# Kernel optimization log

Hardware: AMD Instinct MI355X
Metric: run time of the kernel (lower is better)

Reference implementation:

```python
import jax, jax.numpy as jnp
import numpy as np

DIM = 128
HEADS = 4
CH = DIM // HEADS  # out_channels per head = 32
EDGE_DIM = 1
N_NODES = 50000
N_EDGES = 800000
NEG_SLOPE = 0.2
LN_EPS = 1e-5
SM_EPS = 1e-16  # PyG softmax denom eps


def setup_inputs() -> dict:
    key = jax.random.key(0)
    ks = jax.random.split(key, 10)
    x = jax.random.normal(ks[0], (N_NODES, DIM), dtype=jnp.float32)
    edge_index = jax.random.randint(ks[1], (2, N_EDGES), 0, N_NODES, dtype=jnp.int64)
    edge_attr = jax.random.normal(ks[2], (N_EDGES, EDGE_DIM), dtype=jnp.float32)
    s = 0.05
    W_l = jax.random.normal(ks[3], (DIM, HEADS * CH), dtype=jnp.float32) * s   # shared lin_l/lin_r (share_weights=True)
    b_l = jax.random.normal(ks[4], (HEADS * CH,), dtype=jnp.float32) * s
    W_e = jax.random.normal(ks[5], (EDGE_DIM, HEADS * CH), dtype=jnp.float32) * s  # lin_edge (no bias)
    att = jax.random.normal(ks[6], (HEADS, CH), dtype=jnp.float32) * s
    bias = jax.random.normal(ks[7], (HEADS * CH,), dtype=jnp.float32) * s      # conv output bias
    ln_gamma = jnp.ones((DIM,), dtype=jnp.float32)
    ln_beta = jnp.zeros((DIM,), dtype=jnp.float32)
    return {"x": x, "edge_index": edge_index, "edge_attr": edge_attr,
            "W_l": W_l, "b_l": b_l, "W_e": W_e, "att": att, "bias": bias,
            "ln_gamma": ln_gamma, "ln_beta": ln_beta}


def reference(x, edge_index, edge_attr, W_l, b_l, W_e, att, bias, ln_gamma, ln_beta):
    N = x.shape[0]
    src, dst = edge_index[0], edge_index[1]

    # --- GATv2Conv (share_weights=True, add_self_loops=False, edge_dim injection) ---
    xl = (x @ W_l + b_l).reshape(N, HEADS, CH)            # [N,H,C] (x_l == x_r)
    e = (edge_attr @ W_e).reshape(-1, HEADS, CH)          # [E,H,C]
    m = jax.nn.leaky_relu(xl[src] + xl[dst] + e, NEG_SLOPE)  # [E,H,C]
    alpha = jnp.einsum('ehc,hc->eh', m, att)              # [E,H]

    # segment softmax over destination node neighborhoods
    amax = jax.ops.segment_max(alpha, dst, num_segments=N)   # [N,H]
    ea = jnp.exp(alpha - amax[dst])                           # [E,H]
    denom = jax.ops.segment_sum(ea, dst, num_segments=N)      # [N,H]
    alpha = ea / (denom[dst] + SM_EPS)

    # scatter-aggregate: sum alpha * x_j (projected source feats)
    out = jax.ops.segment_sum(alpha[:, :, None] * xl[src], dst, num_segments=N)  # [N,H,C]
    h = out.reshape(N, HEADS * CH) + bias                  # concat heads + bias -> [N,dim]

    # --- LayerNorm -> GELU (exact, torch default) -> Dropout(eval=identity) -> residual ---
    mu = h.mean(axis=-1, keepdims=True)
    var = ((h - mu) ** 2).mean(axis=-1, keepdims=True)
    hn = (h - mu) * jax.lax.rsqrt(var + LN_EPS) * ln_gamma + ln_beta
    h = jax.nn.gelu(hn, approximate=False)
    return x + h
```

## Files before the change

kernel.cpp:

```cpp
#include <hip/hip_runtime.h>
#include <hip/hip_bf16.h>
#include <stdint.h>


typedef short bf16x8 __attribute__((ext_vector_type(8)));
typedef float f32x4  __attribute__((ext_vector_type(4)));

__device__ __forceinline__ unsigned int f2bf(float f)
{
    __hip_bfloat16 h = __float2bfloat16(f);
    unsigned short u;
    __builtin_memcpy(&u, &h, 2);
    return (unsigned int)u;
}

__global__ void fill_kernel(float* out, int n, float v)
{
    int i = blockIdx.x * 256 + threadIdx.x;
    if (i < n) out[i] = v;
}

__global__ __launch_bounds__(256) void gemm_xl_kernel(
    const float* __restrict__ x, const float* __restrict__ W,
    const float* __restrict__ b, unsigned int* __restrict__ xl, int N)
{
    __shared__ __align__(16) unsigned short sWt[128 * 136];
    __shared__ __align__(16) unsigned short sOut[4 * 16 * 136];
    int tid = threadIdx.x;

    {
        int c  = tid & 127;
        int kh = tid >> 7;
        const float* Wc = W + (size_t)kh * 64 * 128 + c;
        unsigned short* dst = sWt + c * 136 + kh * 64;
#pragma unroll 4
        for (int kk = 0; kk < 16; ++kk) {
            float w0 = Wc[(kk * 4 + 0) * 128];
            float w1 = Wc[(kk * 4 + 1) * 128];
            float w2 = Wc[(kk * 4 + 2) * 128];
            float w3 = Wc[(kk * 4 + 3) * 128];
            uint2 p;
            p.x = f2bf(w0) | (f2bf(w1) << 16);
            p.y = f2bf(w2) | (f2bf(w3) << 16);
            *(uint2*)(dst + kk * 4) = p;
        }
    }
    __syncthreads();

    int w = tid >> 6, lane = tid & 63;
    int li = lane & 15, g = lane >> 4;
    int n0 = blockIdx.x * 128 + w * 32;

    f32x4 acc[2][8];
#pragma unroll
    for (int nt = 0; nt < 8; ++nt) {
        float bb = b[nt * 16 + li];
#pragma unroll
        for (int mt = 0; mt < 2; ++mt) {
            acc[mt][nt][0] = bb; acc[mt][nt][1] = bb;
            acc[mt][nt][2] = bb; acc[mt][nt][3] = bb;
        }
    }

    int row0 = n0 + li;        if (row0 >= N) row0 = N - 1;
    int row1 = n0 + 16 + li;   if (row1 >= N) row1 = N - 1;
    const float* xr0 = x + (size_t)row0 * 128 + g * 8;
    const float* xr1 = x + (size_t)row1 * 128 + g * 8;

#pragma unroll
    for (int kb = 0; kb < 4; ++kb) {
        union { uint32_t u[4]; bf16x8 v; } A0, A1;
        {
            float4 a  = *(const float4*)(xr0 + kb * 32);
            float4 bq = *(const float4*)(xr0 + kb * 32 + 4);
            A0.u[0] = f2bf(a.x)  | (f2bf(a.y)  << 16);
            A0.u[1] = f2bf(a.z)  | (f2bf(a.w)  << 16);
            A0.u[2] = f2bf(bq.x) | (f2bf(bq.y) << 16);
            A0.u[3] = f2bf(bq.z) | (f2bf(bq.w) << 16);
        }
        {
            float4 a  = *(const float4*)(xr1 + kb * 32);
            float4 bq = *(const float4*)(xr1 + kb * 32 + 4);
            A1.u[0] = f2bf(a.x)  | (f2bf(a.y)  << 16);
            A1.u[1] = f2bf(a.z)  | (f2bf(a.w)  << 16);
            A1.u[2] = f2bf(bq.x) | (f2bf(bq.y) << 16);
            A1.u[3] = f2bf(bq.z) | (f2bf(bq.w) << 16);
        }
        const unsigned short* wb = sWt + kb * 32 + g * 8;
#pragma unroll
        for (int nt = 0; nt < 8; ++nt) {
            bf16x8 Bf = *(const bf16x8*)(wb + (nt * 16 + li) * 136);
            acc[0][nt] = __builtin_amdgcn_mfma_f32_16x16x32_bf16(A0.v, Bf, acc[0][nt], 0, 0, 0);
            acc[1][nt] = __builtin_amdgcn_mfma_f32_16x16x32_bf16(A1.v, Bf, acc[1][nt], 0, 0, 0);
        }
    }

    unsigned short* so = sOut + w * 16 * 136;
#pragma unroll
    for (int mt = 0; mt < 2; ++mt) {
#pragma unroll
        for (int nt = 0; nt < 8; ++nt)
#pragma unroll
            for (int r = 0; r < 4; ++r)
                so[(g * 4 + r) * 136 + nt * 16 + li] =
                    (unsigned short)f2bf(acc[mt][nt][r]);
        int rb = n0 + mt * 16;
        for (int it = 0; it < 16; ++it) {
            int n = rb + it;
            if (n < N)
                xl[(size_t)n * 64 + lane] = *(const uint32_t*)(so + it * 136 + lane * 2);
        }
    }
}

__global__ void rank_kernel(const int* __restrict__ ei, int* __restrict__ deg,
                            int* __restrict__ rank, int E, int N)
{
    int e = blockIdx.x * 256 + threadIdx.x;
    if (e < E) {
        int d = ei[(size_t)E + e];
        if ((unsigned)d >= (unsigned)N) d = 0;
        rank[e] = atomicAdd(&deg[d], 1);
    }
}

__global__ void scan_reduce_kernel(const int* __restrict__ deg, int* __restrict__ bsum, int n)
{
    __shared__ int sm[1024];
    int tid = threadIdx.x;
    int i = blockIdx.x * 1024 + tid;
    sm[tid] = (i < n) ? deg[i] : 0;
    __syncthreads();
    for (int o = 512; o >= 1; o >>= 1) {
        if (tid < o) sm[tid] += sm[tid + o];
        __syncthreads();
    }
    if (tid == 0) bsum[blockIdx.x] = sm[0];
}

__global__ __launch_bounds__(1024) void scan_final_kernel(
    const int* __restrict__ deg, const int* __restrict__ bsum,
    int* __restrict__ row_ptr, int n, int E)
{
    __shared__ int sm[1024];
    __shared__ int base;
    int tid = threadIdx.x;
    if (tid == 0) {
        int acc = 0;
        int nb = (int)blockIdx.x;
        for (int i = 0; i < nb; ++i) acc += bsum[i];
        base = acc;
        if (nb == 0) row_ptr[n] = E;
    }
    int i = blockIdx.x * 1024 + tid;
    int v = (i < n) ? deg[i] : 0;
    sm[tid] = v;
    __syncthreads();
    for (int o = 1; o < 1024; o <<= 1) {
        int t = (tid >= o) ? sm[tid - o] : 0;
        __syncthreads();
        sm[tid] += t;
        __syncthreads();
    }
    if (i < n)
        row_ptr[i] = base + sm[tid] - v;
}

__global__ void scatter_kernel(const int* __restrict__ ei, const float* __restrict__ eattr,
                               const int* __restrict__ row_ptr, const int* __restrict__ rank,
                               int2* __restrict__ rec, int E, int N)
{
    int e = blockIdx.x * 256 + threadIdx.x;
    if (e < E) {
        int s = ei[e];
        int d = ei[(size_t)E + e];
        if ((unsigned)d >= (unsigned)N) d = 0;
        int p = row_ptr[d] + rank[e];
        rec[p] = make_int2(s, __float_as_int(eattr[e]));
    }
}

#define SWZ_ADD(p, pat) ((p) + __int_as_float(__builtin_amdgcn_ds_swizzle(__float_as_int(p), (pat))))
#define DPP_ADD(p, ctrl) ((p) + __int_as_float(__builtin_amdgcn_update_dpp(0, __float_as_int(p), (ctrl), 0xF, 0xF, true)))

__global__ void node_kernel(const unsigned int* __restrict__ xlu, const float* __restrict__ x,
                            const int* __restrict__ row_ptr, const int2* __restrict__ rec,
                            const float* __restrict__ We, const float* __restrict__ att,
                            const float* __restrict__ bias, const float* __restrict__ gamma,
                            const float* __restrict__ beta,
                            float2* __restrict__ out, int N)
{
    int gid = blockIdx.x * 256 + threadIdx.x;
    int n = gid >> 6, lane = gid & 63;
    if (n >= N) return;
    int nw = __builtin_amdgcn_readfirstlane(n);
    int r0 = __builtin_amdgcn_readfirstlane(row_ptr[nw]);
    int r1 = __builtin_amdgcn_readfirstlane(row_ptr[nw + 1]);
    int cnt = r1 - r0;
    const int2* rp = rec + r0;

    int c0 = lane * 2;
    const float LOG2E = 1.4426950408889634f;
    float attv0 = att[c0] * LOG2E, attv1 = att[c0 + 1] * LOG2E;
    float wev0 = We[c0],  wev1 = We[c0 + 1];

    unsigned int un = xlu[((unsigned)nw << 6) + lane];
    float b0 = __uint_as_float(un << 16);
    float b1 = __uint_as_float(un & 0xffff0000u);

    float dsA = 0.f, acA0 = 0.f, acA1 = 0.f;
    float dsB = 0.f, acB0 = 0.f, acB1 = 0.f;

    auto edge = [&](unsigned u, float ev, float& ds, float& a0c, float& a1c) {
        float a0 = __uint_as_float(u << 16);
        float a1 = __uint_as_float(u & 0xffff0000u);
        float m0 = a0 + fmaf(ev, wev0, b0);
        float m1 = a1 + fmaf(ev, wev1, b1);
        m0 = fmaf(0.4f, fabsf(m0), 0.6f * m0);
        m1 = fmaf(0.4f, fabsf(m1), 0.6f * m1);
        float p = fmaf(m0, attv0, m1 * attv1);
        p = DPP_ADD(p, 0xB1);
        p = DPP_ADD(p, 0x4E);
        p = DPP_ADD(p, 0x141);
        p = DPP_ADD(p, 0x140);
        float e = __builtin_amdgcn_exp2f(p);
        ds += e;
        a0c = fmaf(e, a0, a0c);
        a1c = fmaf(e, a1, a1c);
    };

    int2 q0, q1, q2, q3;
    if (cnt > 0) {
        q0 = rp[0]; q1 = rp[1]; q2 = rp[2]; q3 = rp[3];
    }
    int t = 0;
    for (; t + 4 <= cnt; t += 4) {
        int   s0 = __builtin_amdgcn_readfirstlane(q0.x);
        float v0 = __int_as_float(__builtin_amdgcn_readfirstlane(q0.y));
        int   s1 = __builtin_amdgcn_readfirstlane(q1.x);
        float v1 = __int_as_float(__builtin_amdgcn_readfirstlane(q1.y));
        int   s2 = __builtin_amdgcn_readfirstlane(q2.x);
        float v2 = __int_as_float(__builtin_amdgcn_readfirstlane(q2.y));
        int   s3 = __builtin_amdgcn_readfirstlane(q3.x);
        float v3 = __int_as_float(__builtin_amdgcn_readfirstlane(q3.y));
        q0 = rp[t + 4]; q1 = rp[t + 5]; q2 = rp[t + 6]; q3 = rp[t + 7];
        unsigned u0 = xlu[(((unsigned)s0) << 6) + lane];
        unsigned u1 = xlu[(((unsigned)s1) << 6) + lane];
        unsigned u2 = xlu[(((unsigned)s2) << 6) + lane];
        unsigned u3 = xlu[(((unsigned)s3) << 6) + lane];
        edge(u0, v0, dsA, acA0, acA1);
        edge(u1, v1, dsB, acB0, acB1);
        edge(u2, v2, dsA, acA0, acA1);
        edge(u3, v3, dsB, acB0, acB1);
    }
    for (; t < cnt; ++t) {
        int2 q = rp[t];
        int   s = __builtin_amdgcn_readfirstlane(q.x);
        float v = __int_as_float(__builtin_amdgcn_readfirstlane(q.y));
        unsigned u = xlu[(((unsigned)s) << 6) + lane];
        edge(u, v, dsA, acA0, acA1);
    }
    float dsum = dsA + dsB;
    float acc0 = acA0 + acB0, acc1 = acA1 + acB1;
    float rdh = 1.f / (dsum + 1e-16f);

    float h0 = acc0 * rdh + bias[c0];
    float h1 = acc1 * rdh + bias[c0 + 1];
    float s1 = h0 + h1, s2 = h0 * h0 + h1 * h1;
    s1 = DPP_ADD(s1, 0xB1);   s2 = DPP_ADD(s2, 0xB1);
    s1 = DPP_ADD(s1, 0x4E);   s2 = DPP_ADD(s2, 0x4E);
    s1 = DPP_ADD(s1, 0x141);  s2 = DPP_ADD(s2, 0x141);
    s1 = DPP_ADD(s1, 0x140);  s2 = DPP_ADD(s2, 0x140);
    s1 = SWZ_ADD(s1, 0x401F); s2 = SWZ_ADD(s2, 0x401F);
    s1 += __shfl_xor(s1, 32);
    s2 += __shfl_xor(s2, 32);
    float mu = s1 * (1.f / 128.f);
    float var = s2 * (1.f / 128.f) - mu * mu;
    var = var < 0.f ? 0.f : var;
    float rstd = rsqrtf(var + 1e-5f);
    float g0 = (h0 - mu) * rstd * gamma[c0]     + beta[c0];
    float g1 = (h1 - mu) * rstd * gamma[c0 + 1] + beta[c0 + 1];
    g0 = 0.5f * g0 * (1.f + erff(g0 * 0.70710678118654752f));
    g1 = 0.5f * g1 * (1.f + erff(g1 * 0.70710678118654752f));

    float2 xin = ((const float2*)x)[(size_t)n * 64 + lane];
    float2 o;
    o.x = xin.x + g0;
    o.y = xin.y + g1;
    out[(size_t)n * 64 + lane] = o;
}

extern "C" void kernel_launch(void* const* d_in, const int* in_sizes, int n_in,
                              void* d_out, int out_size, void* d_ws, size_t ws_size,
                              hipStream_t stream)
{
    const int expect[10] = {6400000, 1600000, 800000, 16384, 128, 128, 128, 128, 128, 128};
    int bad = -1;
    if (n_in != 10) bad = 14;
    else for (int i = 0; i < 10; ++i) if (in_sizes[i] != expect[i]) { bad = i; break; }
    if (bad >= 0) {
        fill_kernel<<<(out_size + 255) / 256, 256, 0, stream>>>((float*)d_out, out_size,
                                                                10000.f + 1000.f * (float)bad);
        return;
    }

    const float* x     = (const float*)d_in[0];
    const int*   ei    = (const int*)d_in[1];
    const float* eattr = (const float*)d_in[2];
    const float* W_l   = (const float*)d_in[3];
    const float* b_l   = (const float*)d_in[4];
    const float* W_e   = (const float*)d_in[5];
    const float* att   = (const float*)d_in[6];
    const float* bias  = (const float*)d_in[7];
    const float* gamma = (const float*)d_in[8];
    const float* beta  = (const float*)d_in[9];

    int N = in_sizes[0] / 128;
    int E = in_sizes[1] / 2;
    int nb = (N + 1023) / 1024;

    uint8_t* w = (uint8_t*)d_ws;
    size_t off = 0;
    unsigned int* xl = (unsigned int*)(w + off); off += (size_t)N * 64 * 4;   off = (off + 255) & ~255ull;
    int* deg     = (int*)(w + off);   off += (size_t)N * 4;        off = (off + 255) & ~255ull;
    int* row_ptr = (int*)(w + off);   off += (size_t)(N + 1) * 4;  off = (off + 255) & ~255ull;
    int* rank    = (int*)(w + off);   off += (size_t)E * 4;        off = (off + 255) & ~255ull;
    int2* rec    = (int2*)(w + off);  off += (size_t)(E + 8) * 8;  off = (off + 255) & ~255ull;
    int* bsum    = (int*)(w + off);   off += (size_t)nb * 4;       off = (off + 255) & ~255ull;

    if (ws_size < off) {
        hipMemsetAsync(d_out, 0, (size_t)out_size * 4, stream);
        return;
    }

    hipMemsetAsync(deg, 0, (size_t)N * 4, stream);
    gemm_xl_kernel<<<(N + 127) / 128, 256, 0, stream>>>(x, W_l, b_l, xl, N);
    rank_kernel<<<(E + 255) / 256, 256, 0, stream>>>(ei, deg, rank, E, N);
    scan_reduce_kernel<<<nb, 1024, 0, stream>>>(deg, bsum, N);
    scan_final_kernel<<<nb, 1024, 0, stream>>>(deg, bsum, row_ptr, N, E);
    scatter_kernel<<<(E + 255) / 256, 256, 0, stream>>>(ei, eattr, row_ptr, rank, rec, E, N);
    node_kernel<<<(N + 3) / 4, 256, 0, stream>>>(xl, x, row_ptr, rec,
                                                 W_e, att, bias, gamma, beta,
                                                 (float2*)d_out, N);
}
```

Measured before the change: 201.6 us.

## Process two edges per wavefront using half-waves with 4 channels per lane

Restructures the node kernel so each half-wavefront (32 lanes) handles a different edge, with each lane owning 4 channels loaded as uint2. Each gather is then 8 bytes per lane, and the head reduction drops one DPP step because 8 lanes now cover a head. The half-wave partial sums are combined with a cross-half shuffle at the end. The scalar remainder loop is replaced by masked paired passes, and the scatter kernel now zero-fills the padding records that those passes may read. This aims to halve the per-edge instruction count and issue wider loads, at the cost of idle lanes during the final store and some tail masking work.

```diff
diff --git a/kernel.cpp b/kernel.cpp
--- a/kernel.cpp
+++ b/kernel.cpp
@@ -177,56 +177,76 @@
         if ((unsigned)d >= (unsigned)N) d = 0;
         int p = row_ptr[d] + rank[e];
         rec[p] = make_int2(s, __float_as_int(eattr[e]));
+    } else if (e < E + 8) {
+        rec[e] = make_int2(0, 0);
     }
 }
 
 #define SWZ_ADD(p, pat) ((p) + __int_as_float(__builtin_amdgcn_ds_swizzle(__float_as_int(p), (pat))))
 #define DPP_ADD(p, ctrl) ((p) + __int_as_float(__builtin_amdgcn_update_dpp(0, __float_as_int(p), (ctrl), 0xF, 0xF, true)))
+#define RFL(v) __builtin_amdgcn_readfirstlane(v)
 
 __global__ void node_kernel(const unsigned int* __restrict__ xlu, const float* __restrict__ x,
                             const int* __restrict__ row_ptr, const int2* __restrict__ rec,
                             const float* __restrict__ We, const float* __restrict__ att,
                             const float* __restrict__ bias, const float* __restrict__ gamma,
                             const float* __restrict__ beta,
-                            float2* __restrict__ out, int N)
+                            float4* __restrict__ out, int N)
 {
     int gid = blockIdx.x * 256 + threadIdx.x;
     int n = gid >> 6, lane = gid & 63;
     if (n >= N) return;
-    int nw = __builtin_amdgcn_readfirstlane(n);
-    int r0 = __builtin_amdgcn_readfirstlane(row_ptr[nw]);
-    int r1 = __builtin_amdgcn_readfirstlane(row_ptr[nw + 1]);
+    int nw = RFL(n);
+    int r0 = RFL(row_ptr[nw]);
+    int r1 = RFL(row_ptr[nw + 1]);
     int cnt = r1 - r0;
     const int2* rp = rec + r0;
 
-    int c0 = lane * 2;
+    int sl  = lane & 31;
+    bool hi = lane >= 32;
+    int c0  = sl * 4;
+    int sl2 = sl * 2;
+
     const float LOG2E = 1.4426950408889634f;
-    float attv0 = att[c0] * LOG2E, attv1 = att[c0 + 1] * LOG2E;
-    float wev0 = We[c0],  wev1 = We[c0 + 1];
-
-    unsigned int un = xlu[((unsigned)nw << 6) + lane];
-    float b0 = __uint_as_float(un << 16);
-    float b1 = __uint_as_float(un & 0xffff0000u);
-
-    float dsA = 0.f, acA0 = 0.f, acA1 = 0.f;
-    float dsB = 0.f, acB0 = 0.f, acB1 = 0.f;
-
-    auto edge = [&](unsigned u, float ev, float& ds, float& a0c, float& a1c) {
-        float a0 = __uint_as_float(u << 16);
-        float a1 = __uint_as_float(u & 0xffff0000u);
-        float m0 = a0 + fmaf(ev, wev0, b0);
-        float m1 = a1 + fmaf(ev, wev1, b1);
+    float4 atq = *(const float4*)(att + c0);
+    float at0 = atq.x * LOG2E, at1 = atq.y * LOG2E;
+    float at2 = atq.z * LOG2E, at3 = atq.w * LOG2E;
+    float4 weq = *(const float4*)(We + c0);
+
+    uint2 un = *(const uint2*)(xlu + (((unsigned)nw) << 6) + sl2);
+    float b0 = __uint_as_float(un.x << 16);
+    float b1 = __uint_as_float(un.x & 0xffff0000u);
+    float b2 = __uint_as_float(un.y << 16);
+    float b3 = __uint_as_float(un.y & 0xffff0000u);
+
+    float ds = 0.f, ac0 = 0.f, ac1 = 0.f, ac2 = 0.f, ac3 = 0.f;
+
+    auto pass_m = [&](int sA, float evA, int sB, float evB, float mA, float mB,
+                      bool masked) {
+        int sv    = hi ? sB : sA;
+        float evv = hi ? evB : evA;
+        uint2 u = *(const uint2*)(xlu + (((unsigned)sv) << 6) + sl2);
+        float a0 = __uint_as_float(u.x << 16);
+        float a1 = __uint_as_float(u.x & 0xffff0000u);
+        float a2 = __uint_as_float(u.y << 16);
+        float a3 = __uint_as_float(u.y & 0xffff0000u);
+        float m0 = a0 + fmaf(evv, weq.x, b0);
+        float m1 = a1 + fmaf(evv, weq.y, b1);
+        float m2 = a2 + fmaf(evv, weq.z, b2);
+        float m3 = a3 + fmaf(evv, weq.w, b3);
         m0 = fmaf(0.4f, fabsf(m0), 0.6f * m0);
         m1 = fmaf(0.4f, fabsf(m1), 0.6f * m1);
-        float p = fmaf(m0, attv0, m1 * attv1);
+        m2 = fmaf(0.4f, fabsf(m2), 0.6f * m2);
+        m3 = fmaf(0.4f, fabsf(m3), 0.6f * m3);
+        float p = fmaf(m0, at0, fmaf(m1, at1, fmaf(m2, at2, m3 * at3)));
         p = DPP_ADD(p, 0xB1);
         p = DPP_ADD(p, 0x4E);
         p = DPP_ADD(p, 0x141);
-        p = DPP_ADD(p, 0x140);
         float e = __builtin_amdgcn_exp2f(p);
+        if (masked) e *= hi ? mB : mA;
         ds += e;
-        a0c = fmaf(e, a0, a0c);
-        a1c = fmaf(e, a1, a1c);
+        ac0 = fmaf(e, a0, ac0); ac1 = fmaf(e, a1, ac1);
+        ac2 = fmaf(e, a2, ac2); ac3 = fmaf(e, a3, ac3);
     };
 
     int2 q0, q1, q2, q3;
@@ -235,59 +255,70 @@
     }
     int t = 0;
     for (; t + 4 <= cnt; t += 4) {
-        int   s0 = __builtin_amdgcn_readfirstlane(q0.x);
-        float v0 = __int_as_float(__builtin_amdgcn_readfirstlane(q0.y));
-        int   s1 = __builtin_amdgcn_readfirstlane(q1.x);
-        float v1 = __int_as_float(__builtin_amdgcn_readfirstlane(q1.y));
-        int   s2 = __builtin_amdgcn_readfirstlane(q2.x);
-        float v2 = __int_as_float(__builtin_amdgcn_readfirstlane(q2.y));
-        int   s3 = __builtin_amdgcn_readfirstlane(q3.x);
-        float v3 = __int_as_float(__builtin_amdgcn_readfirstlane(q3.y));
+        int   s0 = RFL(q0.x); float v0 = __int_as_float(RFL(q0.y));
+        int   s1 = RFL(q1.x); float v1 = __int_as_float(RFL(q1.y));
+        int   s2 = RFL(q2.x); float v2 = __int_as_float(RFL(q2.y));
+        int   s3 = RFL(q3.x); float v3 = __int_as_float(RFL(q3.y));
         q0 = rp[t + 4]; q1 = rp[t + 5]; q2 = rp[t + 6]; q3 = rp[t + 7];
-        unsigned u0 = xlu[(((unsigned)s0) << 6) + lane];
-        unsigned u1 = xlu[(((unsigned)s1) << 6) + lane];
-        unsigned u2 = xlu[(((unsigned)s2) << 6) + lane];
-        unsigned u3 = xlu[(((unsigned)s3) << 6) + lane];
-        edge(u0, v0, dsA, acA0, acA1);
-        edge(u1, v1, dsB, acB0, acB1);
-        edge(u2, v2, dsA, acA0, acA1);
-        edge(u3, v3, dsB, acB0, acB1);
-    }
-    for (; t < cnt; ++t) {
-        int2 q = rp[t];
-        int   s = __builtin_amdgcn_readfirstlane(q.x);
-        float v = __int_as_float(__builtin_amdgcn_readfirstlane(q.y));
-        unsigned u = xlu[(((unsigned)s) << 6) + lane];
-        edge(u, v, dsA, acA0, acA1);
-    }
-    float dsum = dsA + dsB;
-    float acc0 = acA0 + acB0, acc1 = acA1 + acB1;
-    float rdh = 1.f / (dsum + 1e-16f);
-
-    float h0 = acc0 * rdh + bias[c0];
-    float h1 = acc1 * rdh + bias[c0 + 1];
-    float s1 = h0 + h1, s2 = h0 * h0 + h1 * h1;
+        pass_m(s0, v0, s1, v1, 1.f, 1.f, false);
+        pass_m(s2, v2, s3, v3, 1.f, 1.f, false);
+    }
+    int r = cnt - t;
+    if (r > 0) {
+        int   s0 = RFL(q0.x); float v0 = __int_as_float(RFL(q0.y));
+        int   s1 = RFL(q1.x); float v1 = __int_as_float(RFL(q1.y));
+        pass_m(s0, v0, s1, v1, 1.f, (r > 1) ? 1.f : 0.f, true);
+        if (r > 2) {
+            int   s2 = RFL(q2.x); float v2 = __int_as_float(RFL(q2.y));
+            int   s3 = RFL(q3.x); float v3 = __int_as_float(RFL(q3.y));
+            pass_m(s2, v2, s3, v3, 1.f, (r > 3) ? 1.f : 0.f, true);
+        }
+    }
+
+    ds  += __shfl_xor(ds, 32);
+    ac0 += __shfl_xor(ac0, 32);
+    ac1 += __shfl_xor(ac1, 32);
+    ac2 += __shfl_xor(ac2, 32);
+    ac3 += __shfl_xor(ac3, 32);
+    float rdh = 1.f / (ds + 1e-16f);
+
+    float4 biq = *(const float4*)(bias + c0);
+    float h0 = ac0 * rdh + biq.x;
+    float h1 = ac1 * rdh + biq.y;
+    float h2 = ac2 * rdh + biq.z;
+    float h3 = ac3 * rdh + biq.w;
+    float s1 = (h0 + h1) + (h2 + h3);
+    float s2 = fmaf(h0, h0, fmaf(h1, h1, fmaf(h2, h2, h3 * h3)));
     s1 = DPP_ADD(s1, 0xB1);   s2 = DPP_ADD(s2, 0xB1);
     s1 = DPP_ADD(s1, 0x4E);   s2 = DPP_ADD(s2, 0x4E);
     s1 = DPP_ADD(s1, 0x141);  s2 = DPP_ADD(s2, 0x141);
     s1 = DPP_ADD(s1, 0x140);  s2 = DPP_ADD(s2, 0x140);
     s1 = SWZ_ADD(s1, 0x401F); s2 = SWZ_ADD(s2, 0x401F);
-    s1 += __shfl_xor(s1, 32);
-    s2 += __shfl_xor(s2, 32);
     float mu = s1 * (1.f / 128.f);
     float var = s2 * (1.f / 128.f) - mu * mu;
     var = var < 0.f ? 0.f : var;
     float rstd = rsqrtf(var + 1e-5f);
-    float g0 = (h0 - mu) * rstd * gamma[c0]     + beta[c0];
-    float g1 = (h1 - mu) * rstd * gamma[c0 + 1] + beta[c0 + 1];
-    g0 = 0.5f * g0 * (1.f + erff(g0 * 0.70710678118654752f));
-    g1 = 0.5f * g1 * (1.f + erff(g1 * 0.70710678118654752f));
-
-    float2 xin = ((const float2*)x)[(size_t)n * 64 + lane];
-    float2 o;
-    o.x = xin.x + g0;
-    o.y = xin.y + g1;
-    out[(size_t)n * 64 + lane] = o;
+    float4 gaq = *(const float4*)(gamma + c0);
+    float4 beq = *(const float4*)(beta + c0);
+    float g0 = (h0 - mu) * rstd * gaq.x + beq.x;
+    float g1 = (h1 - mu) * rstd * gaq.y + beq.y;
+    float g2 = (h2 - mu) * rstd * gaq.z + beq.z;
+    float g3 = (h3 - mu) * rstd * gaq.w + beq.w;
+    const float IS2 = 0.70710678118654752f;
+    g0 = 0.5f * g0 * (1.f + erff(g0 * IS2));
+    g1 = 0.5f * g1 * (1.f + erff(g1 * IS2));
+    g2 = 0.5f * g2 * (1.f + erff(g2 * IS2));
+    g3 = 0.5f * g3 * (1.f + erff(g3 * IS2));
+
+    if (!hi) {
+        float4 xin = ((const float4*)x)[(size_t)n * 32 + sl];
+        float4 o;
+        o.x = xin.x + g0;
+        o.y = xin.y + g1;
+        o.z = xin.z + g2;
+        o.w = xin.w + g3;
+        out[(size_t)n * 32 + sl] = o;
+    }
 }
 
 extern "C" void kernel_launch(void* const* d_in, const int* in_sizes, int n_in,
@@ -338,8 +369,8 @@
     rank_kernel<<<(E + 255) / 256, 256, 0, stream>>>(ei, deg, rank, E, N);
     scan_reduce_kernel<<<nb, 1024, 0, stream>>>(deg, bsum, N);
     scan_final_kernel<<<nb, 1024, 0, stream>>>(deg, bsum, row_ptr, N, E);
-    scatter_kernel<<<(E + 255) / 256, 256, 0, stream>>>(ei, eattr, row_ptr, rank, rec, E, N);
-    node_kernel<<<(N + 3) / 4, 256, 0, stream>>>(xl, x, row_ptr, rec,
+    scatter_kernel<<<(E + 8 + 255) / 256, 256, 0, stream>>>(ei, eattr, row_ptr, rank, rec, E, N);
+    node_kernel<<<(N + 3) / 4, 256, 0, stream>>>((const unsigned int*)xl, x, row_ptr, rec,
                                                  W_e, att, bias, gamma, beta,
-                                                 (float2*)d_out, N);
-}
+                                                 (float4*)d_out, N);
+}
```

After: 203.2 us. Within noise of the previous version (+0.8%).
